# Performance work log

Measured on AMD Instinct MI355X. Metric: run time of the kernel, lower is better.

## Reference

```python
import jax, jax.numpy as jnp
import numpy as np

EPS = 1.1920929e-07  # torch RMSNorm default eps = finfo(fp32).eps


def _rmsnorm(x, w):
    return x * jax.lax.rsqrt(jnp.mean(x * x, axis=-1, keepdims=True) + EPS) * w


def setup_inputs() -> dict:
    B, S, D, H, SD = 2, 2048, 1024, 16, 64
    ks = jax.random.split(jax.random.key(0), 16)
    scale = 0.02
    return {
        "x": jax.random.normal(ks[0], (B, S, D), jnp.float32),
        "gamma": jax.random.normal(ks[1], (1, 1, D), jnp.float32),
        "beta": jax.random.normal(ks[2], (1, 1, D), jnp.float32),
        "state": jax.random.normal(ks[3], (B, SD), jnp.float32),
        # weights stored as (in, out) so y = x @ W
        "w_qkv": jax.random.normal(ks[4], (D, 3 * D), jnp.float32) * scale,
        "w_o": jax.random.normal(ks[5], (D, D), jnp.float32) * scale,
        "w_gate": jax.random.normal(ks[6], (D, 3 * D), jnp.float32) * scale,
        "w_up": jax.random.normal(ks[7], (D, 3 * D), jnp.float32) * scale,
        "w_down": jax.random.normal(ks[8], (3 * D, D), jnp.float32) * scale,
        "norm1_w": jnp.ones((D,), jnp.float32),
        "norm2_w": jnp.ones((D,), jnp.float32),
        "w_state_mod": jax.random.normal(ks[9], (SD, 2 * D), jnp.float32) * scale,
        "w_h2s": jax.random.normal(ks[10], (D, SD), jnp.float32) * scale,
        "w_sgate": jax.random.normal(ks[11], (2 * SD, SD), jnp.float32) * scale,
    }


def reference(x, gamma, beta, state, w_qkv, w_o, w_gate, w_up, w_down,
              norm1_w, norm2_w, w_state_mod, w_h2s, w_sgate):
    B, S, D = x.shape
    H = 16
    hd = D // H

    # state-conditioned FiLM modulation
    state_mod = state @ w_state_mod                      # (B, 2D)
    state_gamma = 1.0 + state_mod[:, :D][:, None, :]     # (B, 1, D)
    state_beta = state_mod[:, D:][:, None, :]
    full_gamma = gamma * state_gamma
    full_beta = beta + state_beta

    # attention branch
    h = _rmsnorm(x, norm1_w) * full_gamma + full_beta
    qkv = (h @ w_qkv).reshape(B, S, 3, H, hd)
    q = qkv[:, :, 0].transpose(0, 2, 1, 3)               # (B, H, S, hd)
    k = qkv[:, :, 1].transpose(0, 2, 1, 3)
    v = qkv[:, :, 2].transpose(0, 2, 1, 3)
    scores = jnp.einsum('bhqd,bhkd->bhqk', q, k) / np.sqrt(hd).astype(np.float32)
    causal = jnp.tril(jnp.ones((S, S), bool))
    scores = jnp.where(causal, scores, -jnp.inf)
    attn = jax.nn.softmax(scores, axis=-1)
    out = jnp.einsum('bhqk,bhkd->bhqd', attn, v).transpose(0, 2, 1, 3).reshape(B, S, D)
    x = x + out @ w_o

    # SwiGLU FFN branch (same FiLM params)
    h2 = _rmsnorm(x, norm2_w) * full_gamma + full_beta
    gate = jax.nn.silu(h2 @ w_gate)
    x = x + (gate * (h2 @ w_up)) @ w_down

    # recurrent state update
    new_info = jnp.mean(x, axis=1) @ w_h2s               # (B, SD)
    update_gate = jax.nn.sigmoid(jnp.concatenate([state, new_info], axis=-1) @ w_sgate)
    new_state = state * (1.0 - update_gate) + new_info * update_gate
    return x, new_state
```

## Files before the change

kernel.cpp:

```cpp
#include <hip/hip_runtime.h>
#include <hip/hip_bf16.h>

#define EPS_RMS 1.1920929e-07f

constexpr int B_ = 2, S_ = 2048, D_ = 1024, H_ = 16, HD_ = 64, SD_ = 64;
constexpr int M_ = B_ * S_;
constexpr int D3_ = 3 * D_;
constexpr int NT2_ = 512 * 512;

using short8 = __attribute__((ext_vector_type(8))) short;
using f32x4  = __attribute__((ext_vector_type(4))) float;
using f32x16 = __attribute__((ext_vector_type(16))) float;
typedef int v2i __attribute__((ext_vector_type(2)));

static __device__ __forceinline__ ushort f2bf(float x) {
  __hip_bfloat16 h = __float2bfloat16(x);
  return *reinterpret_cast<ushort*>(&h);
}
static __device__ __forceinline__ float bf2f(ushort u) {
  __hip_bfloat16 h;
  *reinterpret_cast<ushort*>(&h) = u;
  return __bfloat162float(h);
}
static __device__ __forceinline__ unsigned pk2(float lo, float hi) {
  return (unsigned)f2bf(lo) | ((unsigned)f2bf(hi) << 16);
}
static __device__ __forceinline__ v2i swap32(int a, int b) {
  return __builtin_amdgcn_permlane32_swap(a, b, false, false);
}
struct alignas(8) bf4 { ushort a, b, c, d; };

static __device__ __forceinline__ void gload16(const ushort* g, ushort* l) {
  __builtin_amdgcn_global_load_lds(
      (const __attribute__((address_space(1))) unsigned int*)g,
      (__attribute__((address_space(3))) unsigned int*)l, 16, 0, 0);
}

__global__ void film_kernel(const float* __restrict__ state,
                            const float* __restrict__ w_sm,
                            const float* __restrict__ gamma,
                            const float* __restrict__ beta,
                            float* __restrict__ fg, float* __restrict__ fb) {
  int c = blockIdx.x * 256 + threadIdx.x;
  int b = blockIdx.y;
  float acc = 0.f;
#pragma unroll 8
  for (int k = 0; k < SD_; ++k)
    acc += state[b * SD_ + k] * w_sm[k * (2 * D_) + c];
  if (c < D_) fg[b * D_ + c] = gamma[c] * (1.f + acc);
  else        fb[b * D_ + (c - D_)] = beta[c - D_] + acc;
}

__global__ __launch_bounds__(256) void rmsnorm_film_kernel(
    const float* __restrict__ X, const float* __restrict__ nw,
    const float* __restrict__ fg, const float* __restrict__ fb,
    ushort* __restrict__ Hout) {
  int row = blockIdx.x;
  int b = row / S_;
  int t = threadIdx.x;
  const float4* x4 = (const float4*)(X + (size_t)row * D_);
  float4 xv = x4[t];
  float ss = xv.x * xv.x + xv.y * xv.y + xv.z * xv.z + xv.w * xv.w;
#pragma unroll
  for (int off = 32; off >= 1; off >>= 1) ss += __shfl_xor(ss, off);
  __shared__ float red[4];
  if ((t & 63) == 0) red[t >> 6] = ss;
  __syncthreads();
  float tot = red[0] + red[1] + red[2] + red[3];
  float scale = rsqrtf(tot / (float)D_ + EPS_RMS);
  int d = t * 4;
  const float4 nw4 = *(const float4*)(nw + d);
  const float4 g4  = *(const float4*)(fg + b * D_ + d);
  const float4 b4  = *(const float4*)(fb + b * D_ + d);
  bf4 hv;
  hv.a = f2bf(xv.x * scale * nw4.x * g4.x + b4.x);
  hv.b = f2bf(xv.y * scale * nw4.y * g4.y + b4.y);
  hv.c = f2bf(xv.z * scale * nw4.z * g4.z + b4.z);
  hv.d = f2bf(xv.w * scale * nw4.w * g4.w + b4.w);
  *(bf4*)(Hout + (size_t)row * D_ + d) = hv;
}

__global__ __launch_bounds__(256) void transpose_bf16(
    const float* __restrict__ W, ushort* __restrict__ Wt, int K, int N) {
  __shared__ float tile[32][33];
  int n0 = blockIdx.x * 32, k0 = blockIdx.y * 32;
  int t = threadIdx.x;
  int c = t & 31, r = t >> 5;
#pragma unroll
  for (int p = 0; p < 4; ++p)
    tile[r + 8 * p][c] = W[(size_t)(k0 + r + 8 * p) * N + n0 + c];
  __syncthreads();
#pragma unroll
  for (int p = 0; p < 4; ++p)
    Wt[(size_t)(n0 + r + 8 * p) * K + k0 + c] = f2bf(tile[c][r + 8 * p]);
}

__global__ __launch_bounds__(256) void transpose_bf16_dual(
    const float* __restrict__ W0, ushort* __restrict__ T0,
    const float* __restrict__ W1, ushort* __restrict__ T1, int K, int N) {
  const float* W = blockIdx.z ? W1 : W0;
  ushort* Wt = blockIdx.z ? T1 : T0;
  __shared__ float tile[32][33];
  int n0 = blockIdx.x * 32, k0 = blockIdx.y * 32;
  int t = threadIdx.x;
  int c = t & 31, r = t >> 5;
#pragma unroll
  for (int p = 0; p < 4; ++p)
    tile[r + 8 * p][c] = W[(size_t)(k0 + r + 8 * p) * N + n0 + c];
  __syncthreads();
#pragma unroll
  for (int p = 0; p < 4; ++p)
    Wt[(size_t)(n0 + r + 8 * p) * K + k0 + c] = f2bf(tile[c][r + 8 * p]);
}

static __device__ __forceinline__ void mfma_tile(
    const char* Au, const char* Bu, f32x4 (&acc)[4][4],
    int l15, int l4, int swz, int wr, int wc) {
#pragma unroll
  for (int kk = 0; kk < 2; ++kk) {
    int tslot = ((kk * 4 + l4) ^ swz) << 4;
    short8 a[4], b[4];
#pragma unroll
    for (int i = 0; i < 4; ++i) {
      int arow = wr * 64 + i * 16 + l15;
      int brow = wc * 64 + i * 16 + l15;
      a[i] = *(const short8*)(Au + arow * 128 + tslot);
      b[i] = *(const short8*)(Bu + brow * 128 + tslot);
    }
#pragma unroll
    for (int m = 0; m < 4; ++m)
#pragma unroll
      for (int n = 0; n < 4; ++n)
        acc[m][n] = __builtin_amdgcn_mfma_f32_16x16x32_bf16(a[m], b[n], acc[m][n], 0, 0, 0);
  }
}

static __device__ __forceinline__ void block_swizzle(int bid, int M, int N,
                                                     int& bm, int& bn) {
  int nbn = N >> 7;
  int nb  = nbn * (M >> 7);
  int qx  = nb >> 3;
  int lin = (bid & 7) * qx + (bid >> 3);
  int grp = lin / (nbn << 3), rem = lin % (nbn << 3);
  bm = ((grp << 3) + (rem & 7)) << 7;
  bn = (rem >> 3) << 7;
}

template<int EPI>
__global__ __launch_bounds__(256, 4) void gemm_mfma(
    const ushort* __restrict__ A, const ushort* __restrict__ Bt,
    const float* __restrict__ Res,
    float* __restrict__ Cf, ushort* __restrict__ Cb, ushort* __restrict__ VtP,
    int M, int N, int K) {
  __shared__ ushort smem[16384];
  char* Au = (char*)smem;
  char* Bu = (char*)(smem + 8192);
  int t = threadIdx.x;
  int bm, bn;
  block_swizzle(blockIdx.x, M, N, bm, bn);

  int lane = t & 63, wid = t >> 6;
  int wr = wid >> 1, wc = wid & 1;
  int l15 = lane & 15, l4 = lane >> 4;
  int swz = l15 & 7;

  const ushort* gA[4];
  const ushort* gB[4];
  ushort* lA[4];
  ushort* lB[4];
#pragma unroll
  for (int p = 0; p < 4; ++p) {
    int seg = p * 4 + wid;
    int flat = seg * 64 + lane;
    int row = flat >> 3, sl = flat & 7;
    int gc = ((sl ^ (row & 7)) << 3);
    gA[p] = A  + (size_t)(bm + row) * K + gc;
    gB[p] = Bt + (size_t)(bn + row) * K + gc;
    lA[p] = smem + seg * 512;
    lB[p] = smem + 8192 + seg * 512;
  }

  f32x4 acc[4][4];
#pragma unroll
  for (int m = 0; m < 4; ++m)
#pragma unroll
    for (int n = 0; n < 4; ++n) acc[m][n] = (f32x4){0.f, 0.f, 0.f, 0.f};

  int nk = K >> 6;
  for (int kt = 0; kt < nk; ++kt) {
    __syncthreads();
#pragma unroll
    for (int p = 0; p < 4; ++p) {
      gload16(gA[p], lA[p]);
      gload16(gB[p], lB[p]);
      gA[p] += 64; gB[p] += 64;
    }
    __syncthreads();
    mfma_tile(Au, Bu, acc, l15, l4, swz, wr, wc);
  }

  if constexpr (EPI == 3) {
#pragma unroll
    for (int m = 0; m < 4; ++m)
#pragma unroll
      for (int n = 0; n < 4; ++n) {
        int row0 = bm + wr * 64 + m * 16 + l4 * 4;
        int col  = bn + wc * 64 + n * 16 + l15;
#pragma unroll
        for (int j = 0; j < 4; ++j) {
          size_t idx = (size_t)(row0 + j) * (size_t)N + col;
          Cf[idx] = Res[idx] + acc[m][n][j];
        }
      }
  } else {
    __syncthreads();
    ushort* Es = smem;
    bool vblk = (bn >= 2048);
#pragma unroll
    for (int m = 0; m < 4; ++m)
#pragma unroll
      for (int n = 0; n < 4; ++n) {
        int rb0 = wr * 64 + m * 16 + l4 * 4;
        int c   = wc * 64 + n * 16 + l15;
#pragma unroll
        for (int j = 0; j < 4; ++j) {
          float v = acc[m][n][j];
          int r = rb0 + j;
          if (vblk) Es[c * 128 + (r ^ ((c & 15) << 3))] = f2bf(v);
          else      Es[r * 128 + c] = f2bf(v);
        }
      }
    __syncthreads();
    if (vblk) {
#pragma unroll
      for (int p = 0; p < 8; ++p) {
        int flat = p * 256 + t;
        int c = flat >> 4, r8 = (flat & 15) * 8;
        int vc = bn - 2048 + c, hh = vc >> 6, dd = vc & 63;
        int bbv = bm >> 11, s0 = (bm & 2047) + r8;
        *(short8*)(VtP + ((((size_t)bbv * 16 + hh) * 64 + dd) << 11) + s0) =
            *(const short8*)&Es[c * 128 + (r8 ^ ((c & 15) << 3))];
      }
    } else {
#pragma unroll
      for (int p = 0; p < 8; ++p) {
        int flat = p * 256 + t;
        int r = flat >> 4, c8 = (flat & 15) * 8;
        *(short8*)(Cb + (size_t)(bm + r) * N + bn + c8) = *(const short8*)&Es[r * 128 + c8];
      }
    }
  }
}

__global__ __launch_bounds__(256, 2) void gemm_dual(
    const ushort* __restrict__ A, const ushort* __restrict__ Gt,
    const ushort* __restrict__ Ut, ushort* __restrict__ Cb,
    int M, int N, int K) {
  __shared__ ushort smem[24576];
  char* Au = (char*)smem;
  char* Gu = (char*)(smem + 8192);
  char* Uu = (char*)(smem + 16384);
  int t = threadIdx.x;
  int bm, bn;
  block_swizzle(blockIdx.x, M, N, bm, bn);

  int lane = t & 63, wid = t >> 6;
  int wr = wid >> 1, wc = wid & 1;
  int l15 = lane & 15, l4 = lane >> 4;
  int swz = l15 & 7;

  const ushort* gA[4]; const ushort* gG[4]; const ushort* gU[4];
  ushort* lA[4]; ushort* lG[4]; ushort* lU[4];
#pragma unroll
  for (int p = 0; p < 4; ++p) {
    int seg = p * 4 + wid;
    int flat = seg * 64 + lane;
    int row = flat >> 3, sl = flat & 7;
    int gc = ((sl ^ (row & 7)) << 3);
    gA[p] = A  + (size_t)(bm + row) * K + gc;
    gG[p] = Gt + (size_t)(bn + row) * K + gc;
    gU[p] = Ut + (size_t)(bn + row) * K + gc;
    lA[p] = smem + seg * 512;
    lG[p] = smem + 8192 + seg * 512;
    lU[p] = smem + 16384 + seg * 512;
  }

  f32x4 ag[4][4], au[4][4];
#pragma unroll
  for (int m = 0; m < 4; ++m)
#pragma unroll
    for (int n = 0; n < 4; ++n) {
      ag[m][n] = (f32x4){0.f, 0.f, 0.f, 0.f};
      au[m][n] = (f32x4){0.f, 0.f, 0.f, 0.f};
    }

  int nk = K >> 6;
  for (int kt = 0; kt < nk; ++kt) {
    __syncthreads();
#pragma unroll
    for (int p = 0; p < 4; ++p) {
      gload16(gA[p], lA[p]);
      gload16(gG[p], lG[p]);
      gload16(gU[p], lU[p]);
      gA[p] += 64; gG[p] += 64; gU[p] += 64;
    }
    __syncthreads();
#pragma unroll
    for (int kk = 0; kk < 2; ++kk) {
      int tslot = ((kk * 4 + l4) ^ swz) << 4;
      short8 a[4], bg[4], bu[4];
#pragma unroll
      for (int i = 0; i < 4; ++i) {
        int arow = wr * 64 + i * 16 + l15;
        int brow = wc * 64 + i * 16 + l15;
        a[i]  = *(const short8*)(Au + arow * 128 + tslot);
        bg[i] = *(const short8*)(Gu + brow * 128 + tslot);
        bu[i] = *(const short8*)(Uu + brow * 128 + tslot);
      }
#pragma unroll
      for (int m = 0; m < 4; ++m)
#pragma unroll
        for (int n = 0; n < 4; ++n) {
          ag[m][n] = __builtin_amdgcn_mfma_f32_16x16x32_bf16(a[m], bg[n], ag[m][n], 0, 0, 0);
          au[m][n] = __builtin_amdgcn_mfma_f32_16x16x32_bf16(a[m], bu[n], au[m][n], 0, 0, 0);
        }
    }
  }

  __syncthreads();
  ushort* Es = smem;
#pragma unroll
  for (int m = 0; m < 4; ++m)
#pragma unroll
    for (int n = 0; n < 4; ++n) {
      int rb0 = wr * 64 + m * 16 + l4 * 4;
      int c   = wc * 64 + n * 16 + l15;
#pragma unroll
      for (int j = 0; j < 4; ++j) {
        float gv = ag[m][n][j];
        float v = gv / (1.f + __expf(-gv)) * au[m][n][j];
        Es[(rb0 + j) * 128 + c] = f2bf(v);
      }
    }
  __syncthreads();
#pragma unroll
  for (int p = 0; p < 8; ++p) {
    int flat = p * 256 + t;
    int r = flat >> 4, c8 = (flat & 15) * 8;
    *(short8*)(Cb + (size_t)(bm + r) * N + bn + c8) = *(const short8*)&Es[r * 128 + c8];
  }
}

__global__ __launch_bounds__(512, 4) void attn_mfma_kernel(
    const ushort* __restrict__ qkv,
    const ushort* __restrict__ Vt,
    unsigned* __restrict__ PO,
    float* __restrict__ PM, float* __restrict__ PL) {
  __shared__ ushort lds[16384];
  const float SL2 = 0.125f * 1.44269504f;
  int t = threadIdx.x;
  int x = blockIdx.x;
  int lin = ((x & 7) << 6) + (x >> 3);
  int kh = lin & 1;
  int pp = (lin >> 1) & 7;
  int hb = lin >> 4;
  int h = hb & 15, bb = hb >> 4;
  int lane = t & 63, wv = t >> 6;
  int qi = wv >> 2, wsub = wv & 3;
  int qt = qi ? (15 - pp) : pp;
  int q0 = qt * 128;
  int l31 = lane & 31, g = lane >> 5;

  int qrow = q0 + wsub * 32 + l31;
  const ushort* qrow_ptr = qkv + (size_t)(bb * S_ + qrow) * 3072 + h * 64;
  short8 qf[4];
#pragma unroll
  for (int s = 0; s < 4; ++s) qf[s] = *(const short8*)(qrow_ptr + s * 16 + g * 8);

  f32x16 accO[2];
#pragma unroll
  for (int u = 0; u < 2; ++u)
#pragma unroll
    for (int r = 0; r < 16; ++r) accO[u][r] = 0.f;
  float m = -INFINITY, l = 0.f;
  int qg = qrow;
  int qmin = q0 + wsub * 32, qmax = qmin + 31;
  int ntpair = 2 * (16 - pp);
  int ntk = (ntpair - kh + 1) >> 1;

  const ushort* kbase = qkv + (size_t)(bb * S_) * 3072 + 1024 + h * 64;
  const ushort* vbase = Vt + ((size_t)(bb * 16 + h) * 64) * 2048;

  int srow = t >> 3, sslot = t & 7;
  int soff = srow * 64 + ((sslot ^ (srow & 7)) << 3);
  const ushort* kg0 = kbase + (size_t)srow * 3072 + sslot * 8;
  const ushort* vg0 = vbase + (size_t)srow * 2048 + sslot * 8;

  *(short8*)&lds[soff] = *(const short8*)(kg0 + (size_t)kh * (64 * 3072));
  *(short8*)&lds[4096 + soff] = *(const short8*)(vg0 + kh * 64);
  __syncthreads();

  for (int i2 = 0; i2 < ntk; ++i2) {
    int cur = i2 & 1;
    int kti = 2 * i2 + kh;
    int kt = kti << 6;
    bool pf = (i2 + 1 < ntk);
    short8 rk, rv;
    if (pf) {
      rk = *(const short8*)(kg0 + (size_t)(kti + 2) * (64 * 3072));
      rv = *(const short8*)(vg0 + (kti + 2) * 64);
    }
    if (kt <= qmax) {
      const ushort* Kb = lds + cur * 8192;
      const ushort* Vb = Kb + 4096;

      f32x16 accT[2];
#pragma unroll
      for (int t2 = 0; t2 < 2; ++t2)
#pragma unroll
        for (int r = 0; r < 16; ++r) accT[t2][r] = 0.f;
      __builtin_amdgcn_s_setprio(1);
#pragma unroll
      for (int t2 = 0; t2 < 2; ++t2) {
        int key = 32 * t2 + l31;
#pragma unroll
        for (int s = 0; s < 4; ++s) {
          short8 kf = *(const short8*)&Kb[key * 64 + (((2 * s + g) ^ (key & 7)) << 3)];
          accT[t2] = __builtin_amdgcn_mfma_f32_32x32x16_bf16(kf, qf[s], accT[t2], 0, 0, 0);
        }
      }
      __builtin_amdgcn_s_setprio(0);

      bool need_mask = (kt + 63 > qmin);
      float p_[2][16];
      float pmax = -INFINITY;
#pragma unroll
      for (int t2 = 0; t2 < 2; ++t2)
#pragma unroll
        for (int r = 0; r < 16; ++r) {
          float v = accT[t2][r] * SL2;
          if (need_mask) {
            int key = kt + 32 * t2 + (r & 3) + 8 * (r >> 2) + 4 * g;
            if (key > qg) v = -INFINITY;
          }
          p_[t2][r] = v;
          pmax = fmaxf(pmax, v);
        }
      {
        v2i pm = swap32(__float_as_int(pmax), __float_as_int(pmax));
        pmax = fmaxf(pmax, __int_as_float(g ? pm.x : pm.y));
      }

      if (__any(pmax > m + 11.5f)) {
        float mnew = fmaxf(m, pmax);
        float corr = exp2f(m - mnew);
        m = mnew;
        l *= corr;
        float cr[16];
#pragma unroll
        for (int r = 0; r < 16; ++r) cr[r] = __shfl(corr, (r & 3) + 8 * (r >> 2) + 4 * g);
#pragma unroll
        for (int r = 0; r < 16; ++r) { accO[0][r] *= cr[r]; accO[1][r] *= cr[r]; }
      }
      float psum = 0.f;
#pragma unroll
      for (int t2 = 0; t2 < 2; ++t2)
#pragma unroll
        for (int r = 0; r < 16; ++r) {
          float e = exp2f(p_[t2][r] - m);
          p_[t2][r] = e;
          psum += e;
        }
      {
        v2i ps = swap32(__float_as_int(psum), __float_as_int(psum));
        psum += __int_as_float(g ? ps.x : ps.y);
      }
      l += psum;

#pragma unroll
      for (int s = 0; s < 4; ++s) {
        int ca = 2 * s, cb2 = 2 * s + 1;
        int ta = ca >> 2, ra = (ca & 3) * 4;
        int tb = cb2 >> 2, rbq = (cb2 & 3) * 4;
        int w0a = (int)pk2(p_[ta][ra], p_[ta][ra + 1]);
        int w1a = (int)pk2(p_[ta][ra + 2], p_[ta][ra + 3]);
        int w0b = (int)pk2(p_[tb][rbq], p_[tb][rbq + 1]);
        int w1b = (int)pk2(p_[tb][rbq + 2], p_[tb][rbq + 3]);
        v2i r0 = swap32(w0a, w0b);
        v2i r1 = swap32(w1a, w1b);
        union { int u[4]; short8 s8; } pa;
        pa.u[0] = r0.x;
        pa.u[1] = r1.x;
        pa.u[2] = r0.y;
        pa.u[3] = r1.y;
        __builtin_amdgcn_s_setprio(1);
#pragma unroll
        for (int u = 0; u < 2; ++u) {
          int d = 32 * u + l31;
          short8 vf = *(const short8*)&Vb[d * 64 + (((2 * s + g) ^ (d & 7)) << 3)];
          accO[u] = __builtin_amdgcn_mfma_f32_32x32x16_bf16(pa.s8, vf, accO[u], 0, 0, 0);
        }
        __builtin_amdgcn_s_setprio(0);
      }
    }
    if (pf) {
      ushort* dst = lds + (cur ^ 1) * 8192;
      *(short8*)&dst[soff] = rk;
      *(short8*)&dst[4096 + soff] = rv;
    }
    __syncthreads();
  }

  size_t base = (size_t)lin * 512 + t;
#pragma unroll
  for (int r = 0; r < 16; ++r)
    PO[(size_t)r * NT2_ + base] = pk2(accO[0][r], accO[1][r]);
  PM[base] = m;
  PL[base] = l;
}

__global__ __launch_bounds__(512, 2) void attn_merge_kernel(
    const unsigned* __restrict__ PO, const float* __restrict__ PM,
    const float* __restrict__ PL, ushort* __restrict__ AO) {
  __shared__ ushort lds[16384];
  int t = threadIdx.x;
  int xb = blockIdx.x;
  int lin2 = ((xb & 7) << 5) + (xb >> 3);
  int pp = lin2 & 7;
  int hb = lin2 >> 3;
  int h = hb & 15, bb = hb >> 4;
  int lane = t & 63, wv = t >> 6;
  int l31 = lane & 31, g = lane >> 5;

  size_t p0 = ((size_t)((hb << 4) | (pp << 1)) * 512) + t;
  size_t p1 = p0 + 512;
  float m0 = PM[p0], l0 = PL[p0];
  float m1 = PM[p1], l1 = PL[p1];
  float mn = fmaxf(m0, m1);
  float c0 = exp2f(m0 - mn), c1 = exp2f(m1 - mn);
  float linv = 1.f / (l0 * c0 + l1 * c1);

  float cr0[16], cr1[16], lr[16];
#pragma unroll
  for (int r = 0; r < 16; ++r) {
    int src = (r & 3) + 8 * (r >> 2) + 4 * g;
    cr0[r] = __shfl(c0, src);
    cr1[r] = __shfl(c1, src);
    lr[r]  = __shfl(linv, src);
  }
#pragma unroll
  for (int r = 0; r < 16; ++r) {
    unsigned u0 = PO[(size_t)r * NT2_ + p0];
    unsigned u1 = PO[(size_t)r * NT2_ + p1];
    float a0 = bf2f((ushort)(u0 & 0xffff)), b0 = bf2f((ushort)(u0 >> 16));
    float a1 = bf2f((ushort)(u1 & 0xffff)), b1 = bf2f((ushort)(u1 >> 16));
    int row = wv * 32 + (r & 3) + 8 * (r >> 2) + 4 * g;
    lds[row * 64 + l31]      = f2bf((a0 * cr0[r] + a1 * cr1[r]) * lr[r]);
    lds[row * 64 + 32 + l31] = f2bf((b0 * cr0[r] + b1 * cr1[r]) * lr[r]);
  }
  __syncthreads();
#pragma unroll
  for (int p = 0; p < 4; ++p) {
    int flat = p * 512 + t;
    int row = flat >> 3, slot = flat & 7;
    int qto = (row < 128) ? pp : (15 - pp);
    int grow = row & 127;
    *(short8*)(AO + (size_t)(bb * S_ + qto * 128 + grow) * 1024 + h * 64 + slot * 8) =
        *(const short8*)&lds[row * 64 + slot * 8];
  }
}

__global__ void colmean1(const float* __restrict__ X, float* __restrict__ part) {
  int d = blockIdx.x * 256 + threadIdx.x;
  int b = blockIdx.y;
  int ch = blockIdx.z;
  float s = 0.f;
  int s0 = ch * (S_ / 16);
  for (int i = 0; i < S_ / 16; ++i)
    s += X[(size_t)(b * S_ + s0 + i) * D_ + d];
  part[(b * 16 + ch) * D_ + d] = s;
}

__global__ __launch_bounds__(1024) void colmean2_state_kernel(
    const float* __restrict__ part, const float* __restrict__ state,
    const float* __restrict__ w_h2s, const float* __restrict__ w_sg,
    float* __restrict__ out_tail) {
  __shared__ float cms[2048];
  __shared__ float nis[128];
  int t = threadIdx.x;
#pragma unroll
  for (int i = 0; i < 2; ++i) {
    int idx = i * 1024 + t;
    int b = idx >> 10, d = idx & 1023;
    float s = 0.f;
#pragma unroll
    for (int c = 0; c < 16; ++c) s += part[(b * 16 + c) * D_ + d];
    cms[idx] = s * (1.f / (float)S_);
  }
  __syncthreads();
  {
    int out = t >> 3, ks = t & 7;
    int b = out >> 6, j = out & 63;
    float ni = 0.f;
    int k0 = ks * 128;
#pragma unroll 8
    for (int k = k0; k < k0 + 128; ++k)
      ni += cms[b * 1024 + k] * w_h2s[k * SD_ + j];
    ni += __shfl_xor(ni, 1);
    ni += __shfl_xor(ni, 2);
    ni += __shfl_xor(ni, 4);
    if (ks == 0) nis[out] = ni;
  }
  __syncthreads();
  if (t < 128) {
    int b = t >> 6, j = t & 63;
    float nv = nis[t];
    float g = 0.f;
#pragma unroll
    for (int k = 0; k < SD_; ++k) g += state[b * SD_ + k] * w_sg[k * SD_ + j];
#pragma unroll
    for (int k = 0; k < SD_; ++k) g += nis[b * SD_ + k] * w_sg[(SD_ + k) * SD_ + j];
    g = 1.f / (1.f + __expf(-g));
    float st = state[b * SD_ + j];
    out_tail[t] = st * (1.f - g) + nv * g;
  }
}

extern "C" void kernel_launch(void* const* d_in, const int* in_sizes, int n_in,
                              void* d_out, int out_size, void* d_ws, size_t ws_size,
                              hipStream_t stream) {
  const float* x      = (const float*)d_in[0];
  const float* gamma  = (const float*)d_in[1];
  const float* beta   = (const float*)d_in[2];
  const float* state  = (const float*)d_in[3];
  const float* w_qkv  = (const float*)d_in[4];
  const float* w_o    = (const float*)d_in[5];
  const float* w_gate = (const float*)d_in[6];
  const float* w_up   = (const float*)d_in[7];
  const float* w_down = (const float*)d_in[8];
  const float* norm1w = (const float*)d_in[9];
  const float* norm2w = (const float*)d_in[10];
  const float* w_sm   = (const float*)d_in[11];
  const float* w_h2s  = (const float*)d_in[12];
  const float* w_sg   = (const float*)d_in[13];
  float* out = (float*)d_out;

  float* ws = (float*)d_ws;
  float*  fg     = ws;
  float*  fb     = ws + 2048;
  float*  part   = ws + 8192;
  ushort* h_bf   = (ushort*)(ws + 65536);
  ushort* wT     = (ushort*)(ws + 65536 + 2097152);
  ushort* wT2    = (ushort*)(ws + 65536 + 3670016);
  unsigned* PO   = (unsigned*)(ws + 65536);
  float*  PM     = ws + 65536 + 4194304;
  float*  PL     = ws + 65536 + 4456448;
  ushort* AO_bf  = (ushort*)(ws + 65536 + 5242880);
  ushort* qkv_bf = (ushort*)(ws + 65536 + 7340032);
  ushort* Vt_g   = (ushort*)(ws + 65536 + 13631488);
  ushort* gu_bf  = qkv_bf;

  film_kernel<<<dim3(8, B_), 256, 0, stream>>>(state, w_sm, gamma, beta, fg, fb);
  rmsnorm_film_kernel<<<M_, 256, 0, stream>>>(x, norm1w, fg, fb, h_bf);
  transpose_bf16<<<dim3(D3_ / 32, D_ / 32), 256, 0, stream>>>(w_qkv, wT, D_, D3_);
  gemm_mfma<4><<<(D3_ / 128) * (M_ / 128), 256, 0, stream>>>(
      h_bf, wT, nullptr, nullptr, qkv_bf, Vt_g, M_, D3_, D_);
  attn_mfma_kernel<<<512, 512, 0, stream>>>(qkv_bf, Vt_g, PO, PM, PL);
  attn_merge_kernel<<<256, 512, 0, stream>>>(PO, PM, PL, AO_bf);
  transpose_bf16<<<dim3(D_ / 32, D_ / 32), 256, 0, stream>>>(w_o, wT, D_, D_);
  gemm_mfma<3><<<(D_ / 128) * (M_ / 128), 256, 0, stream>>>(
      AO_bf, wT, x, out, nullptr, nullptr, M_, D_, D_);
  rmsnorm_film_kernel<<<M_, 256, 0, stream>>>(out, norm2w, fg, fb, h_bf);
  transpose_bf16_dual<<<dim3(D3_ / 32, D_ / 32, 2), 256, 0, stream>>>(
      w_gate, wT, w_up, wT2, D_, D3_);
  gemm_dual<<<(D3_ / 128) * (M_ / 128), 256, 0, stream>>>(
      h_bf, wT, wT2, gu_bf, M_, D3_, D_);
  transpose_bf16<<<dim3(D_ / 32, D3_ / 32), 256, 0, stream>>>(w_down, wT, D3_, D_);
  gemm_mfma<3><<<(D_ / 128) * (M_ / 128), 256, 0, stream>>>(
      gu_bf, wT, out, out, nullptr, nullptr, M_, D_, D3_);
  colmean1<<<dim3(4, B_, 16), 256, 0, stream>>>(out, part);
  colmean2_state_kernel<<<1, 1024, 0, stream>>>(part, state, w_h2s, w_sg,
                                                out + (size_t)M_ * D_);
}
```

Before: 296.1 us.

## Fuse column-sum into down-proj GEMM epilogue and batch w_o transpose

The down-projection GEMM epilogue now sums each output column over its rows and atomically adds the partial into a per-batch column-sum buffer. This replaces the separate colmean1 pass that re-read the full output. The w_o transpose is merged into the w_qkv transpose launch through a generalized dual transpose kernel that writes to a separate buffer, removing one launch. The cost is a memset, atomics in the epilogue, and float summation order that now depends on atomic ordering.

```diff
diff --git a/kernel.cpp b/kernel.cpp
--- a/kernel.cpp
+++ b/kernel.cpp
@@ -95,13 +95,16 @@
     Wt[(size_t)(n0 + r + 8 * p) * K + k0 + c] = f2bf(tile[c][r + 8 * p]);
 }
 
-__global__ __launch_bounds__(256) void transpose_bf16_dual(
-    const float* __restrict__ W0, ushort* __restrict__ T0,
-    const float* __restrict__ W1, ushort* __restrict__ T1, int K, int N) {
+__global__ __launch_bounds__(256) void transpose_bf16_dual2(
+    const float* __restrict__ W0, ushort* __restrict__ T0, int K0, int N0,
+    const float* __restrict__ W1, ushort* __restrict__ T1, int K1, int N1) {
   const float* W = blockIdx.z ? W1 : W0;
   ushort* Wt = blockIdx.z ? T1 : T0;
+  int K = blockIdx.z ? K1 : K0;
+  int N = blockIdx.z ? N1 : N0;
+  int n0 = blockIdx.x * 32, k0 = blockIdx.y * 32;
+  if (n0 >= N || k0 >= K) return;
   __shared__ float tile[32][33];
-  int n0 = blockIdx.x * 32, k0 = blockIdx.y * 32;
   int t = threadIdx.x;
   int c = t & 31, r = t >> 5;
 #pragma unroll
@@ -151,6 +154,7 @@
     const ushort* __restrict__ A, const ushort* __restrict__ Bt,
     const float* __restrict__ Res,
     float* __restrict__ Cf, ushort* __restrict__ Cb, ushort* __restrict__ VtP,
+    float* __restrict__ Csum,
     int M, int N, int K) {
   __shared__ ushort smem[16384];
   char* Au = (char*)smem;
@@ -199,19 +203,25 @@
     mfma_tile(Au, Bu, acc, l15, l4, swz, wr, wc);
   }
 
-  if constexpr (EPI == 3) {
-#pragma unroll
-    for (int m = 0; m < 4; ++m)
-#pragma unroll
-      for (int n = 0; n < 4; ++n) {
+  if constexpr (EPI == 3 || EPI == 5) {
+#pragma unroll
+    for (int n = 0; n < 4; ++n) {
+      int col = bn + wc * 64 + n * 16 + l15;
+      float s = 0.f;
+#pragma unroll
+      for (int m = 0; m < 4; ++m) {
         int row0 = bm + wr * 64 + m * 16 + l4 * 4;
-        int col  = bn + wc * 64 + n * 16 + l15;
 #pragma unroll
         for (int j = 0; j < 4; ++j) {
           size_t idx = (size_t)(row0 + j) * (size_t)N + col;
-          Cf[idx] = Res[idx] + acc[m][n][j];
+          float outv = Res[idx] + acc[m][n][j];
+          Cf[idx] = outv;
+          s += outv;
         }
       }
+      if constexpr (EPI == 5)
+        atomicAdd(&Csum[(bm >> 11) * 1024 + col], s);
+    }
   } else {
     __syncthreads();
     ushort* Es = smem;
@@ -570,19 +580,8 @@
   }
 }
 
-__global__ void colmean1(const float* __restrict__ X, float* __restrict__ part) {
-  int d = blockIdx.x * 256 + threadIdx.x;
-  int b = blockIdx.y;
-  int ch = blockIdx.z;
-  float s = 0.f;
-  int s0 = ch * (S_ / 16);
-  for (int i = 0; i < S_ / 16; ++i)
-    s += X[(size_t)(b * S_ + s0 + i) * D_ + d];
-  part[(b * 16 + ch) * D_ + d] = s;
-}
-
 __global__ __launch_bounds__(1024) void colmean2_state_kernel(
-    const float* __restrict__ part, const float* __restrict__ state,
+    const float* __restrict__ csum, const float* __restrict__ state,
     const float* __restrict__ w_h2s, const float* __restrict__ w_sg,
     float* __restrict__ out_tail) {
   __shared__ float cms[2048];
@@ -591,11 +590,7 @@
 #pragma unroll
   for (int i = 0; i < 2; ++i) {
     int idx = i * 1024 + t;
-    int b = idx >> 10, d = idx & 1023;
-    float s = 0.f;
-#pragma unroll
-    for (int c = 0; c < 16; ++c) s += part[(b * 16 + c) * D_ + d];
-    cms[idx] = s * (1.f / (float)S_);
+    cms[idx] = csum[idx] * (1.f / (float)S_);
   }
   __syncthreads();
   {
@@ -648,7 +643,7 @@
   float* ws = (float*)d_ws;
   float*  fg     = ws;
   float*  fb     = ws + 2048;
-  float*  part   = ws + 8192;
+  float*  csum   = ws + 8192;
   ushort* h_bf   = (ushort*)(ws + 65536);
   ushort* wT     = (ushort*)(ws + 65536 + 2097152);
   ushort* wT2    = (ushort*)(ws + 65536 + 3670016);
@@ -658,27 +653,28 @@
   ushort* AO_bf  = (ushort*)(ws + 65536 + 5242880);
   ushort* qkv_bf = (ushort*)(ws + 65536 + 7340032);
   ushort* Vt_g   = (ushort*)(ws + 65536 + 13631488);
+  ushort* w_oT   = (ushort*)(ws + 65536 + 15728640);
   ushort* gu_bf  = qkv_bf;
 
+  hipMemsetAsync(csum, 0, 2048 * sizeof(float), stream);
   film_kernel<<<dim3(8, B_), 256, 0, stream>>>(state, w_sm, gamma, beta, fg, fb);
   rmsnorm_film_kernel<<<M_, 256, 0, stream>>>(x, norm1w, fg, fb, h_bf);
-  transpose_bf16<<<dim3(D3_ / 32, D_ / 32), 256, 0, stream>>>(w_qkv, wT, D_, D3_);
+  transpose_bf16_dual2<<<dim3(D3_ / 32, D_ / 32, 2), 256, 0, stream>>>(
+      w_qkv, wT, D_, D3_, w_o, w_oT, D_, D_);
   gemm_mfma<4><<<(D3_ / 128) * (M_ / 128), 256, 0, stream>>>(
-      h_bf, wT, nullptr, nullptr, qkv_bf, Vt_g, M_, D3_, D_);
+      h_bf, wT, nullptr, nullptr, qkv_bf, Vt_g, nullptr, M_, D3_, D_);
   attn_mfma_kernel<<<512, 512, 0, stream>>>(qkv_bf, Vt_g, PO, PM, PL);
   attn_merge_kernel<<<256, 512, 0, stream>>>(PO, PM, PL, AO_bf);
-  transpose_bf16<<<dim3(D_ / 32, D_ / 32), 256, 0, stream>>>(w_o, wT, D_, D_);
   gemm_mfma<3><<<(D_ / 128) * (M_ / 128), 256, 0, stream>>>(
-      AO_bf, wT, x, out, nullptr, nullptr, M_, D_, D_);
+      AO_bf, w_oT, x, out, nullptr, nullptr, nullptr, M_, D_, D_);
   rmsnorm_film_kernel<<<M_, 256, 0, stream>>>(out, norm2w, fg, fb, h_bf);
-  transpose_bf16_dual<<<dim3(D3_ / 32, D_ / 32, 2), 256, 0, stream>>>(
-      w_gate, wT, w_up, wT2, D_, D3_);
+  transpose_bf16_dual2<<<dim3(D3_ / 32, D_ / 32, 2), 256, 0, stream>>>(
+      w_gate, wT, D_, D3_, w_up, wT2, D_, D3_);
   gemm_dual<<<(D3_ / 128) * (M_ / 128), 256, 0, stream>>>(
       h_bf, wT, wT2, gu_bf, M_, D3_, D_);
   transpose_bf16<<<dim3(D_ / 32, D3_ / 32), 256, 0, stream>>>(w_down, wT, D3_, D_);
-  gemm_mfma<3><<<(D_ / 128) * (M_ / 128), 256, 0, stream>>>(
-      gu_bf, wT, out, out, nullptr, nullptr, M_, D_, D3_);
-  colmean1<<<dim3(4, B_, 16), 256, 0, stream>>>(out, part);
-  colmean2_state_kernel<<<1, 1024, 0, stream>>>(part, state, w_h2s, w_sg,
+  gemm_mfma<5><<<(D_ / 128) * (M_ / 128), 256, 0, stream>>>(
+      gu_bf, wT, out, out, nullptr, nullptr, csum, M_, D_, D3_);
+  colmean2_state_kernel<<<1, 1024, 0, stream>>>(csum, state, w_h2s, w_sg,
                                                 out + (size_t)M_ * D_);
 }
```

Result: slower. 317.7 us (+7.3%).
